# Performance work log

Hardware: AMD Instinct MI355X
Metric: run time of the kernel (lower is better)

Reference implementation:

```python
import jax, jax.numpy as jnp
import numpy as np

B, T, D = 2, 2048, 2048
N, K, H = 16, 8, 128  # heads, kv heads, head_dim
F = 8192              # ffn hidden


def _apply_rope(x, positions, max_wavelength=10000):
    # x: [B, L, heads, H]; positions: [B, L]
    half = x.shape[-1] // 2
    freq_exponents = (2.0 / x.shape[-1]) * jnp.arange(half, dtype=jnp.float32)
    timescale = max_wavelength ** freq_exponents
    radians = positions.astype(jnp.float32)[..., None] / timescale[None, None, :]
    radians = radians[..., None, :]  # [B, L, 1, half]
    sin, cos = jnp.sin(radians), jnp.cos(radians)
    x1, x2 = jnp.split(x, 2, axis=-1)
    return jnp.concatenate([x1 * cos - x2 * sin, x2 * cos + x1 * sin], axis=-1)


def _rms_norm(x, scale):
    var = jnp.mean(jnp.square(x), axis=-1, keepdims=True)
    return x * jax.lax.rsqrt(var + 1e-6) * (1 + scale)


def setup_inputs() -> dict:
    key = jax.random.key(0)
    ks = jax.random.split(key, 8)
    s = 0.02
    x = jax.random.normal(ks[0], (B, T, D), jnp.float32)
    positions = jnp.broadcast_to(jnp.arange(T, dtype=jnp.int32)[None, :], (B, T))
    causal = jnp.tril(jnp.ones((T, T), dtype=bool))
    attn_mask = jnp.broadcast_to(causal[None, None, :, :], (B, 1, T, T))
    return {
        "x": x,
        "positions": positions,
        "attn_mask": attn_mask,
        "w_q": jax.random.normal(ks[1], (N, D, H), jnp.float32) * s,
        "w_kv": jax.random.normal(ks[2], (2, K, D, H), jnp.float32) * s,
        "w_attn_vec": jax.random.normal(ks[3], (N, H, D), jnp.float32) * s,
        "scale_pre_attn": jax.random.normal(ks[4], (D,), jnp.float32) * s,
        "scale_pre_ffw": jax.random.normal(ks[5], (D,), jnp.float32) * s,
        "w_gating": jax.random.normal(ks[6], (2, D, F), jnp.float32) * s,
        "w_linear": jax.random.normal(ks[7], (F, D), jnp.float32) * s,
    }


def reference(x, positions, attn_mask, w_q, w_kv, w_attn_vec,
              scale_pre_attn, scale_pre_ffw, w_gating, w_linear):
    # pre-attention RMSNorm
    xn = _rms_norm(x, scale_pre_attn)

    # GQA projections
    q = jnp.einsum('BTD,NDH->BTNH', xn, w_q)
    kv = jnp.einsum('BSD,eKDH->eBSKH', xn, w_kv)
    k, v = kv[0], kv[1]

    q = _apply_rope(q, positions) * (H ** -0.5)
    k = _apply_rope(k, positions)

    G = N // K
    q = q.reshape(q.shape[0], q.shape[1], K, G, H)  # B T K G H
    logits = jnp.einsum('BTKGH,BSKH->BKGTS', q, k).astype(jnp.float32)
    big_neg = -2.3819763e38
    masked = jnp.where(attn_mask[:, :, None, :, :], logits, big_neg)
    probs = jax.nn.softmax(masked, axis=-1).astype(k.dtype)
    enc = jnp.einsum('BKGTS,BSKH->BTKGH', probs, v)
    enc = enc.reshape(enc.shape[0], enc.shape[1], N, H)
    attn_out = jnp.einsum('BTNH,NHD->BTD', enc, w_attn_vec)

    # residual + pre-FFN RMSNorm + GeGLU FFN
    residual = x + attn_out
    h = _rms_norm(residual, scale_pre_ffw)
    gate = jax.nn.gelu(jnp.dot(h, w_gating[0]))
    act = gate * jnp.dot(h, w_gating[1])
    out = residual + jnp.dot(act, w_linear)
    return out
```

## Files before the change

### kernel.cpp

```cpp
#include <hip/hip_runtime.h>
#include <hip/hip_bf16.h>


typedef __attribute__((ext_vector_type(8))) short bf16x8;
typedef __attribute__((ext_vector_type(4))) float f32x4;

#define GLP(p) ((const __attribute__((address_space(1))) void*)(p))
#define LDSP(p) ((__attribute__((address_space(3))) void*)(p))

__device__ __forceinline__ float bf2f(unsigned short h) {
  union { unsigned int u; float f; } v; v.u = ((unsigned int)h) << 16; return v.f;
}
__device__ __forceinline__ unsigned short f2bf(float f) {
  union { float f; unsigned int u; } v; v.f = f;
  unsigned int r = v.u + 0x7fffu + ((v.u >> 16) & 1u);
  return (unsigned short)(r >> 16);
}
__device__ __forceinline__ float gelu_f(float x) {
  float t = tanhf(0.7978845608028654f * (x + 0.044715f * x * x * x));
  return 0.5f * x * (1.f + t);
}

template <int IN_F32>
__global__ __launch_bounds__(256) void rmsnorm_kernel(const void* __restrict__ x_,
                                                      const float* __restrict__ scale,
                                                      unsigned short* __restrict__ out) {
  int row = blockIdx.x, tid = threadIdx.x;
  float f[8]; float ss = 0.f;
  if (IN_F32) {
    const float* xr = (const float*)x_ + (size_t)row * 2048 + tid * 8;
#pragma unroll
    for (int i = 0; i < 8; ++i) { f[i] = xr[i]; ss += f[i] * f[i]; }
  } else {
    const unsigned short* xr = (const unsigned short*)x_ + (size_t)row * 2048;
    bf16x8 xv = *(const bf16x8*)(xr + tid * 8);
#pragma unroll
    for (int i = 0; i < 8; ++i) { f[i] = bf2f((unsigned short)xv[i]); ss += f[i] * f[i]; }
  }
#pragma unroll
  for (int off = 32; off >= 1; off >>= 1) ss += __shfl_xor(ss, off);
  __shared__ float red[4];
  if ((tid & 63) == 0) red[tid >> 6] = ss;
  __syncthreads();
  ss = red[0] + red[1] + red[2] + red[3];
  float r = rsqrtf(ss * (1.f / 2048.f) + 1e-6f);
  const float* sv = scale + tid * 8;
  bf16x8 o;
#pragma unroll
  for (int i = 0; i < 8; ++i) o[i] = (short)f2bf(f[i] * r * (1.f + sv[i]));
  *(bf16x8*)(out + (size_t)row * 2048 + tid * 8) = o;
}

__global__ __launch_bounds__(256) void transpose_cast_kernel(const float* __restrict__ in,
                                                             unsigned short* __restrict__ out,
                                                             int R, int ldi, long ibs, long obs) {
  __shared__ float tile[32][33];
  int z = blockIdx.z;
  const float* ip = in + (size_t)z * ibs;
  unsigned short* op = out + (size_t)z * obs;
  int c0 = blockIdx.x * 32, r0 = blockIdx.y * 32;
  int tx = threadIdx.x, ty = threadIdx.y;
#pragma unroll
  for (int i = 0; i < 32; i += 8)
    tile[ty + i][tx] = ip[(size_t)(r0 + ty + i) * ldi + (c0 + tx)];
  __syncthreads();
#pragma unroll
  for (int i = 0; i < 32; i += 8)
    op[(size_t)(c0 + ty + i) * R + (r0 + tx)] = f2bf(tile[tx][ty + i]);
}

__global__ __launch_bounds__(256) void vtrans_kernel(const unsigned short* __restrict__ qkv,
                                                     unsigned short* __restrict__ vT) {
  __shared__ unsigned short tile[32][33];
  int z = blockIdx.z, bb = z >> 3, kh = z & 7;
  int s0 = blockIdx.x * 32, h0 = blockIdx.y * 32;
  int tx = threadIdx.x, ty = threadIdx.y;
  const unsigned short* ip = qkv + ((size_t)bb * 2048) * 4096 + 3072 + kh * 128;
  unsigned short* op = vT + (size_t)z * 128 * 2048;
#pragma unroll
  for (int i = 0; i < 32; i += 8)
    tile[ty + i][tx] = ip[(size_t)(s0 + ty + i) * 4096 + h0 + tx];
  __syncthreads();
#pragma unroll
  for (int i = 0; i < 32; i += 8)
    op[(size_t)(h0 + ty + i) * 2048 + s0 + tx] = tile[tx][ty + i];
}

template <int MODE, int OUT_F32, int ADD_F32>
__global__ __launch_bounds__(256, 2) void gemm_bt(const unsigned short* __restrict__ A, int lda,
                                                  const unsigned short* __restrict__ BT, int Kd,
                                                  int Ncols, void* __restrict__ out_,
                                                  const void* __restrict__ add_) {
  __shared__ unsigned short sA[128 * 32];
  __shared__ unsigned short sB[128 * 32];
  int tid = threadIdx.x;
  int lane = tid & 63, wave = tid >> 6;
  int quad = lane >> 4, l16 = lane & 15;
  int wr = (wave >> 1) * 64, wc = (wave & 1) * 64;
  long rowBase = (long)blockIdx.y * 128, colBase = (long)blockIdx.x * 128;
  f32x4 acc[4][4];
#pragma unroll
  for (int i = 0; i < 4; ++i)
#pragma unroll
    for (int j = 0; j < 4; ++j) acc[i][j] = (f32x4){0.f, 0.f, 0.f, 0.f};

  const unsigned short* Ag = A + (rowBase + (tid >> 2)) * (size_t)lda + (tid & 3) * 8;
  const unsigned short* Bg = BT + (colBase + (tid >> 2)) * (size_t)Kd + (tid & 3) * 8;
  unsigned short* sAw = sA + wave * 512;
  unsigned short* sBw = sB + wave * 512;

  for (int kt = 0; kt < Kd; kt += 32) {
    __syncthreads();
    __builtin_amdgcn_global_load_lds(GLP(Ag), LDSP(sAw), 16, 0, 0);
    __builtin_amdgcn_global_load_lds(GLP(Ag + (size_t)64 * lda), LDSP(sAw + 2048), 16, 0, 0);
    __builtin_amdgcn_global_load_lds(GLP(Bg), LDSP(sBw), 16, 0, 0);
    __builtin_amdgcn_global_load_lds(GLP(Bg + (size_t)64 * Kd), LDSP(sBw + 2048), 16, 0, 0);
    Ag += 32; Bg += 32;
    __syncthreads();
    bf16x8 af[4], bfr[4];
#pragma unroll
    for (int i = 0; i < 4; ++i) af[i] = *(const bf16x8*)(sA + (wr + i * 16 + l16) * 32 + quad * 8);
#pragma unroll
    for (int j = 0; j < 4; ++j) bfr[j] = *(const bf16x8*)(sB + (wc + j * 16 + l16) * 32 + quad * 8);
#pragma unroll
    for (int i = 0; i < 4; ++i)
#pragma unroll
      for (int j = 0; j < 4; ++j)
        acc[i][j] = __builtin_amdgcn_mfma_f32_16x16x32_bf16(af[i], bfr[j], acc[i][j], 0, 0, 0);
  }
  float* outf = (float*)out_;
  unsigned short* outb = (unsigned short*)out_;
  const float* addf = (const float*)add_;
  const unsigned short* addb = (const unsigned short*)add_;
#pragma unroll
  for (int i = 0; i < 4; ++i)
#pragma unroll
    for (int j = 0; j < 4; ++j)
#pragma unroll
      for (int r = 0; r < 4; ++r) {
        long row = rowBase + wr + i * 16 + quad * 4 + r;
        long col = colBase + wc + j * 16 + l16;
        long idx = row * (long)Ncols + col;
        float v = acc[i][j][r];
        if (MODE == 1) v += (ADD_F32 ? addf[idx] : bf2f(addb[idx]));
        if (OUT_F32) outf[idx] = v; else outb[idx] = f2bf(v);
      }
}

__global__ __launch_bounds__(256, 2) void gemm_gating(const unsigned short* __restrict__ A,
                                                      const unsigned short* __restrict__ BgT,
                                                      const unsigned short* __restrict__ BuT,
                                                      unsigned short* __restrict__ act,
                                                      long colOfs) {
  __shared__ unsigned short sA[128 * 32];
  __shared__ unsigned short sBg[128 * 32];
  __shared__ unsigned short sBu[128 * 32];
  int tid = threadIdx.x;
  int lane = tid & 63, wave = tid >> 6;
  int quad = lane >> 4, l16 = lane & 15;
  int wr = (wave >> 1) * 64, wc = (wave & 1) * 64;
  long rowBase = (long)blockIdx.y * 128, colBase = (long)blockIdx.x * 128;
  f32x4 gacc[4][4], uacc[4][4];
#pragma unroll
  for (int i = 0; i < 4; ++i)
#pragma unroll
    for (int j = 0; j < 4; ++j) {
      gacc[i][j] = (f32x4){0.f, 0.f, 0.f, 0.f};
      uacc[i][j] = (f32x4){0.f, 0.f, 0.f, 0.f};
    }

  const unsigned short* Ag  = A + (rowBase + (tid >> 2)) * (size_t)2048 + (tid & 3) * 8;
  const unsigned short* Bgg = BgT + (colBase + (tid >> 2)) * (size_t)2048 + (tid & 3) * 8;
  const unsigned short* Bug = BuT + (colBase + (tid >> 2)) * (size_t)2048 + (tid & 3) * 8;
  unsigned short* sAw = sA + wave * 512;
  unsigned short* sBgw = sBg + wave * 512;
  unsigned short* sBuw = sBu + wave * 512;

  for (int kt = 0; kt < 2048; kt += 32) {
    __syncthreads();
    __builtin_amdgcn_global_load_lds(GLP(Ag), LDSP(sAw), 16, 0, 0);
    __builtin_amdgcn_global_load_lds(GLP(Ag + (size_t)64 * 2048), LDSP(sAw + 2048), 16, 0, 0);
    __builtin_amdgcn_global_load_lds(GLP(Bgg), LDSP(sBgw), 16, 0, 0);
    __builtin_amdgcn_global_load_lds(GLP(Bgg + (size_t)64 * 2048), LDSP(sBgw + 2048), 16, 0, 0);
    __builtin_amdgcn_global_load_lds(GLP(Bug), LDSP(sBuw), 16, 0, 0);
    __builtin_amdgcn_global_load_lds(GLP(Bug + (size_t)64 * 2048), LDSP(sBuw + 2048), 16, 0, 0);
    Ag += 32; Bgg += 32; Bug += 32;
    __syncthreads();
    bf16x8 af[4], bg[4], bu[4];
#pragma unroll
    for (int i = 0; i < 4; ++i) af[i] = *(const bf16x8*)(sA + (wr + i * 16 + l16) * 32 + quad * 8);
#pragma unroll
    for (int j = 0; j < 4; ++j) bg[j] = *(const bf16x8*)(sBg + (wc + j * 16 + l16) * 32 + quad * 8);
#pragma unroll
    for (int j = 0; j < 4; ++j) bu[j] = *(const bf16x8*)(sBu + (wc + j * 16 + l16) * 32 + quad * 8);
#pragma unroll
    for (int i = 0; i < 4; ++i)
#pragma unroll
      for (int j = 0; j < 4; ++j) {
        gacc[i][j] = __builtin_amdgcn_mfma_f32_16x16x32_bf16(af[i], bg[j], gacc[i][j], 0, 0, 0);
        uacc[i][j] = __builtin_amdgcn_mfma_f32_16x16x32_bf16(af[i], bu[j], uacc[i][j], 0, 0, 0);
      }
  }
#pragma unroll
  for (int i = 0; i < 4; ++i)
#pragma unroll
    for (int j = 0; j < 4; ++j)
#pragma unroll
      for (int r = 0; r < 4; ++r) {
        long row = rowBase + wr + i * 16 + quad * 4 + r;
        long col = colBase + wc + j * 16 + l16;
        act[row * 8192 + colOfs + col] = f2bf(gelu_f(gacc[i][j][r]) * uacc[i][j][r]);
      }
}

__global__ __launch_bounds__(256) void rope_kernel(unsigned short* __restrict__ qkv,
                                                   const int* __restrict__ pos) {
  int gid = blockIdx.x * 256 + threadIdx.x;
  int hp = gid & 63;
  int rh = gid >> 6;
  int row = rh / 24;
  int head = rh - row * 24;
  float p = (float)pos[row];
  long cb; float sc;
  if (head < 16) { cb = (long)head * 128; sc = 0.08838834764831845f; }
  else { cb = 2048 + (long)(head - 16) * 128; sc = 1.f; }
  unsigned short* ptr = qkv + (long)row * 4096 + cb;
  float inv = exp2f(-(float)hp * (13.287712379549449f / 64.f));
  float ang = p * inv;
  float s = sinf(ang), c = cosf(ang);
  float x1 = bf2f(ptr[hp]), x2 = bf2f(ptr[hp + 64]);
  ptr[hp]      = f2bf((x1 * c - x2 * s) * sc);
  ptr[hp + 64] = f2bf((x2 * c + x1 * s) * sc);
}

__global__ __launch_bounds__(256, 2) void attn_kernel(const unsigned short* __restrict__ qkv,
                                                      const unsigned short* __restrict__ vT,
                                                      unsigned short* __restrict__ enc) {
  extern __shared__ char smem[];
  unsigned short* sK = (unsigned short*)smem;
  unsigned short* sVT = sK + 64 * 128;
  float* sS = (float*)(smem + 32768);
  unsigned short* sP = (unsigned short*)(smem + 32768 + 16896);
  float* sM = (float*)(smem + 32768 + 16896 + 9216);
  float* sL = sM + 64;
  float* sAl = sL + 64;

  int qt = blockIdx.x, n = blockIdx.y, b = blockIdx.z;
  int tid = threadIdx.x, lane = tid & 63, w = tid >> 6;
  int quad = lane >> 4, l16 = lane & 15;
  int kh = n >> 1;
  long rowQ = (long)b * 2048 + (long)qt * 64;

  bf16x8 qf[4];
  {
    const unsigned short* qp = qkv + (rowQ + w * 16 + l16) * 4096 + n * 128 + quad * 8;
#pragma unroll
    for (int ks = 0; ks < 4; ++ks) qf[ks] = *(const bf16x8*)(qp + ks * 32);
  }
  if (tid < 64) { sM[tid] = -1e30f; sL[tid] = 0.f; }
  f32x4 oacc[8];
#pragma unroll
  for (int t = 0; t < 8; ++t) oacc[t] = (f32x4){0.f, 0.f, 0.f, 0.f};

  int srow = tid >> 2, cg = tid & 3;

  for (int st = 0; st <= qt; ++st) {
    __syncthreads();
#pragma unroll
    for (int it = 0; it < 4; ++it) {
      int idx = it * 256 + tid;
      int r = idx >> 4, c = idx & 15;
      bf16x8 kv8 = *(const bf16x8*)(qkv + ((long)b * 2048 + st * 64 + r) * 4096 + 2048 + kh * 128 + c * 8);
      *(bf16x8*)(sK + r * 128 + ((c ^ (r & 7)) * 8)) = kv8;
    }
#pragma unroll
    for (int it = 0; it < 4; ++it) {
      int idx = it * 256 + tid;
      int h = idx >> 3, c = idx & 7;
      bf16x8 vv8 = *(const bf16x8*)(vT + ((long)(b * 8 + kh) * 128 + h) * 2048 + st * 64 + c * 8);
      *(bf16x8*)(sVT + h * 64 + ((c ^ (h & 7)) * 8)) = vv8;
    }
    __syncthreads();

    f32x4 sacc[4];
#pragma unroll
    for (int nt = 0; nt < 4; ++nt) sacc[nt] = (f32x4){0.f, 0.f, 0.f, 0.f};
#pragma unroll
    for (int ks = 0; ks < 4; ++ks)
#pragma unroll
      for (int nt = 0; nt < 4; ++nt) {
        int r = nt * 16 + l16;
        bf16x8 kf = *(const bf16x8*)(sK + r * 128 + (((ks * 4 + quad) ^ (r & 7)) * 8));
        sacc[nt] = __builtin_amdgcn_mfma_f32_16x16x32_bf16(qf[ks], kf, sacc[nt], 0, 0, 0);
      }
#pragma unroll
    for (int nt = 0; nt < 4; ++nt)
#pragma unroll
      for (int r = 0; r < 4; ++r)
        sS[(w * 16 + quad * 4 + r) * 66 + nt * 16 + l16] = sacc[nt][r];
    __syncthreads();

    float vals[16];
    int tglob = qt * 64 + srow;
    float mx = -1e30f;
#pragma unroll
    for (int j = 0; j < 16; ++j) {
      int col = cg * 16 + j;
      float v = sS[srow * 66 + col];
      if (st * 64 + col > tglob) v = -1e30f;
      vals[j] = v;
      mx = fmaxf(mx, v);
    }
    mx = fmaxf(mx, __shfl_xor(mx, 1));
    mx = fmaxf(mx, __shfl_xor(mx, 2));
    float m_old = sM[srow], l_old = sL[srow];
    float m_new = fmaxf(m_old, mx);
    float alpha = __expf(m_old - m_new);
    float sum = 0.f;
#pragma unroll
    for (int j = 0; j < 16; ++j) { vals[j] = __expf(vals[j] - m_new); sum += vals[j]; }
    sum += __shfl_xor(sum, 1);
    sum += __shfl_xor(sum, 2);
    float l_new = alpha * l_old + sum;
    __syncthreads();

#pragma unroll
    for (int jj = 0; jj < 8; ++jj) {
      unsigned int pk = (unsigned int)f2bf(vals[2 * jj]) | ((unsigned int)f2bf(vals[2 * jj + 1]) << 16);
      *(unsigned int*)(sP + srow * 72 + cg * 16 + jj * 2) = pk;
    }
    if (cg == 0) { sM[srow] = m_new; sL[srow] = l_new; sAl[srow] = alpha; }
    __syncthreads();

#pragma unroll
    for (int r = 0; r < 4; ++r) {
      float al = sAl[w * 16 + quad * 4 + r];
#pragma unroll
      for (int nt = 0; nt < 8; ++nt) oacc[nt][r] *= al;
    }
#pragma unroll
    for (int ks = 0; ks < 2; ++ks) {
      bf16x8 pf = *(const bf16x8*)(sP + (w * 16 + l16) * 72 + ks * 32 + quad * 8);
#pragma unroll
      for (int nt = 0; nt < 8; ++nt) {
        int hh = nt * 16 + l16;
        bf16x8 vf = *(const bf16x8*)(sVT + hh * 64 + (((ks * 4 + quad) ^ (hh & 7)) * 8));
        oacc[nt] = __builtin_amdgcn_mfma_f32_16x16x32_bf16(pf, vf, oacc[nt], 0, 0, 0);
      }
    }
  }

#pragma unroll
  for (int r = 0; r < 4; ++r) {
    float invl = 1.f / sL[w * 16 + quad * 4 + r];
    long trow = rowQ + w * 16 + quad * 4 + r;
#pragma unroll
    for (int nt = 0; nt < 8; ++nt)
      enc[trow * 2048 + n * 128 + nt * 16 + l16] = f2bf(oacc[nt][r] * invl);
  }
}

extern "C" void kernel_launch(void* const* d_in, const int* in_sizes, int n_in,
                              void* d_out, int out_size, void* d_ws, size_t ws_size,
                              hipStream_t stream) {
  const float* x = (const float*)d_in[0];
  const int* positions = (const int*)d_in[1];
  const float* wq = (const float*)d_in[3];
  const float* wkv = (const float*)d_in[4];
  const float* wav = (const float*)d_in[5];
  const float* s_attn = (const float*)d_in[6];
  const float* s_ffw = (const float*)d_in[7];
  const float* wg = (const float*)d_in[8];
  const float* wl = (const float*)d_in[9];
  float* outp = (float*)d_out;

  char* ws = (char*)d_ws;
  size_t o = 0;
  unsigned short* XN = (unsigned short*)(ws + o);    o += (size_t)4096 * 2048 * 2;
  unsigned short* WQKVT = (unsigned short*)(ws + o); o += (size_t)4096 * 2048 * 2;
  unsigned short* WAVT = (unsigned short*)(ws + o);  o += (size_t)2048 * 2048 * 2;
  unsigned short* WGT = (unsigned short*)(ws + o);   o += (size_t)8192 * 2048 * 2;
  unsigned short* QKV = (unsigned short*)(ws + o);   o += (size_t)4096 * 4096 * 2;
  unsigned short* VTb = (unsigned short*)(ws + o);   o += (size_t)16 * 128 * 2048 * 2;
  unsigned short* ACT = (unsigned short*)(ws + o);   o += (size_t)4096 * 8192 * 2;
  unsigned short* ENC = WQKVT;
  unsigned short* RES = QKV;
  unsigned short* HB = XN;

  dim3 b256(256), bT(32, 8);

  rmsnorm_kernel<1><<<4096, b256, 0, stream>>>(x, s_attn, XN);

  transpose_cast_kernel<<<dim3(4, 64, 16), bT, 0, stream>>>(wq, WQKVT, 2048, 128, 262144L, 262144L);
  transpose_cast_kernel<<<dim3(4, 64, 8), bT, 0, stream>>>(wkv, WQKVT + (size_t)2048 * 2048, 2048, 128, 262144L, 262144L);
  transpose_cast_kernel<<<dim3(4, 64, 8), bT, 0, stream>>>(wkv + (size_t)8 * 262144, WQKVT + (size_t)3072 * 2048, 2048, 128, 262144L, 262144L);
  transpose_cast_kernel<<<dim3(64, 64, 1), bT, 0, stream>>>(wav, WAVT, 2048, 2048, 0L, 0L);

  gemm_bt<0, 0, 0><<<dim3(32, 32), b256, 0, stream>>>(XN, 2048, WQKVT, 2048, 4096, QKV, nullptr);

  vtrans_kernel<<<dim3(64, 4, 16), bT, 0, stream>>>(QKV, VTb);

  rope_kernel<<<24576, b256, 0, stream>>>(QKV, positions);

  attn_kernel<<<dim3(32, 16, 2), b256, 59648, stream>>>(QKV, VTb, ENC);

  gemm_bt<1, 0, 1><<<dim3(16, 32), b256, 0, stream>>>(ENC, 2048, WAVT, 2048, 2048, RES, x);

  rmsnorm_kernel<0><<<4096, b256, 0, stream>>>(RES, s_ffw, HB);

  for (int half = 0; half < 2; ++half) {
    long f0 = (long)half * 4096;
    transpose_cast_kernel<<<dim3(128, 64, 1), bT, 0, stream>>>(wg + f0, WGT, 2048, 8192, 0L, 0L);
    transpose_cast_kernel<<<dim3(128, 64, 1), bT, 0, stream>>>(wg + (size_t)2048 * 8192 + f0,
                                                               WGT + (size_t)4096 * 2048, 2048, 8192, 0L, 0L);
    gemm_gating<<<dim3(32, 32), b256, 0, stream>>>(HB, WGT, WGT + (size_t)4096 * 2048, ACT, f0);
  }

  transpose_cast_kernel<<<dim3(64, 256, 1), bT, 0, stream>>>(wl, WGT, 8192, 2048, 0L, 0L);
  gemm_bt<1, 1, 0><<<dim3(16, 32), b256, 0, stream>>>(ACT, 8192, WGT, 8192, 2048, outp, RES);
}
```

Baseline: 1.155 ms.

## Double-buffer LDS tiles in GEMM kernels to overlap loads with MFMA

Both the generic GEMM and the fused gating GEMM now use two LDS buffers per operand. Each block issues the first tile's global-to-LDS load up front. Inside the loop it starts the async load of tile k+1 into the spare buffer before running the MFMAs on tile k, and it drops one of the two barriers per iteration. This is meant to hide global memory latency behind matrix compute, at the cost of doubled LDS per block (48KB for the gating kernel), which could limit occupancy.

```diff
diff --git a/kernel.cpp b/kernel.cpp
--- a/kernel.cpp
+++ b/kernel.cpp
@@ -91,8 +91,8 @@
                                                   const unsigned short* __restrict__ BT, int Kd,
                                                   int Ncols, void* __restrict__ out_,
                                                   const void* __restrict__ add_) {
-  __shared__ unsigned short sA[128 * 32];
-  __shared__ unsigned short sB[128 * 32];
+  __shared__ unsigned short sA0[128 * 32], sA1[128 * 32];
+  __shared__ unsigned short sB0[128 * 32], sB1[128 * 32];
   int tid = threadIdx.x;
   int lane = tid & 63, wave = tid >> 6;
   int quad = lane >> 4, l16 = lane & 15;
@@ -106,27 +106,38 @@
 
   const unsigned short* Ag = A + (rowBase + (tid >> 2)) * (size_t)lda + (tid & 3) * 8;
   const unsigned short* Bg = BT + (colBase + (tid >> 2)) * (size_t)Kd + (tid & 3) * 8;
-  unsigned short* sAw = sA + wave * 512;
-  unsigned short* sBw = sB + wave * 512;
-
-  for (int kt = 0; kt < Kd; kt += 32) {
-    __syncthreads();
-    __builtin_amdgcn_global_load_lds(GLP(Ag), LDSP(sAw), 16, 0, 0);
-    __builtin_amdgcn_global_load_lds(GLP(Ag + (size_t)64 * lda), LDSP(sAw + 2048), 16, 0, 0);
-    __builtin_amdgcn_global_load_lds(GLP(Bg), LDSP(sBw), 16, 0, 0);
-    __builtin_amdgcn_global_load_lds(GLP(Bg + (size_t)64 * Kd), LDSP(sBw + 2048), 16, 0, 0);
-    Ag += 32; Bg += 32;
-    __syncthreads();
+  int wofs = wave * 512;
+
+  __builtin_amdgcn_global_load_lds(GLP(Ag), LDSP(sA0 + wofs), 16, 0, 0);
+  __builtin_amdgcn_global_load_lds(GLP(Ag + (size_t)64 * lda), LDSP(sA0 + 2048 + wofs), 16, 0, 0);
+  __builtin_amdgcn_global_load_lds(GLP(Bg), LDSP(sB0 + wofs), 16, 0, 0);
+  __builtin_amdgcn_global_load_lds(GLP(Bg + (size_t)64 * Kd), LDSP(sB0 + 2048 + wofs), 16, 0, 0);
+  Ag += 32; Bg += 32;
+
+  unsigned short *curA = sA0, *nxtA = sA1, *curB = sB0, *nxtB = sB1;
+  int nIter = Kd >> 5;
+  for (int k = 0; k < nIter; ++k) {
+    __syncthreads();
+    if (k + 1 < nIter) {
+      __builtin_amdgcn_global_load_lds(GLP(Ag), LDSP(nxtA + wofs), 16, 0, 0);
+      __builtin_amdgcn_global_load_lds(GLP(Ag + (size_t)64 * lda), LDSP(nxtA + 2048 + wofs), 16, 0, 0);
+      __builtin_amdgcn_global_load_lds(GLP(Bg), LDSP(nxtB + wofs), 16, 0, 0);
+      __builtin_amdgcn_global_load_lds(GLP(Bg + (size_t)64 * Kd), LDSP(nxtB + 2048 + wofs), 16, 0, 0);
+      Ag += 32; Bg += 32;
+    }
     bf16x8 af[4], bfr[4];
 #pragma unroll
-    for (int i = 0; i < 4; ++i) af[i] = *(const bf16x8*)(sA + (wr + i * 16 + l16) * 32 + quad * 8);
-#pragma unroll
-    for (int j = 0; j < 4; ++j) bfr[j] = *(const bf16x8*)(sB + (wc + j * 16 + l16) * 32 + quad * 8);
+    for (int i = 0; i < 4; ++i) af[i] = *(const bf16x8*)(curA + (wr + i * 16 + l16) * 32 + quad * 8);
+#pragma unroll
+    for (int j = 0; j < 4; ++j) bfr[j] = *(const bf16x8*)(curB + (wc + j * 16 + l16) * 32 + quad * 8);
 #pragma unroll
     for (int i = 0; i < 4; ++i)
 #pragma unroll
       for (int j = 0; j < 4; ++j)
         acc[i][j] = __builtin_amdgcn_mfma_f32_16x16x32_bf16(af[i], bfr[j], acc[i][j], 0, 0, 0);
+    unsigned short* t;
+    t = curA; curA = nxtA; nxtA = t;
+    t = curB; curB = nxtB; nxtB = t;
   }
   float* outf = (float*)out_;
   unsigned short* outb = (unsigned short*)out_;
@@ -152,9 +163,9 @@
                                                       const unsigned short* __restrict__ BuT,
                                                       unsigned short* __restrict__ act,
                                                       long colOfs) {
-  __shared__ unsigned short sA[128 * 32];
-  __shared__ unsigned short sBg[128 * 32];
-  __shared__ unsigned short sBu[128 * 32];
+  __shared__ unsigned short sA0[128 * 32], sA1[128 * 32];
+  __shared__ unsigned short sG0[128 * 32], sG1[128 * 32];
+  __shared__ unsigned short sU0[128 * 32], sU1[128 * 32];
   int tid = threadIdx.x;
   int lane = tid & 63, wave = tid >> 6;
   int quad = lane >> 4, l16 = lane & 15;
@@ -172,27 +183,35 @@
   const unsigned short* Ag  = A + (rowBase + (tid >> 2)) * (size_t)2048 + (tid & 3) * 8;
   const unsigned short* Bgg = BgT + (colBase + (tid >> 2)) * (size_t)2048 + (tid & 3) * 8;
   const unsigned short* Bug = BuT + (colBase + (tid >> 2)) * (size_t)2048 + (tid & 3) * 8;
-  unsigned short* sAw = sA + wave * 512;
-  unsigned short* sBgw = sBg + wave * 512;
-  unsigned short* sBuw = sBu + wave * 512;
-
-  for (int kt = 0; kt < 2048; kt += 32) {
-    __syncthreads();
-    __builtin_amdgcn_global_load_lds(GLP(Ag), LDSP(sAw), 16, 0, 0);
-    __builtin_amdgcn_global_load_lds(GLP(Ag + (size_t)64 * 2048), LDSP(sAw + 2048), 16, 0, 0);
-    __builtin_amdgcn_global_load_lds(GLP(Bgg), LDSP(sBgw), 16, 0, 0);
-    __builtin_amdgcn_global_load_lds(GLP(Bgg + (size_t)64 * 2048), LDSP(sBgw + 2048), 16, 0, 0);
-    __builtin_amdgcn_global_load_lds(GLP(Bug), LDSP(sBuw), 16, 0, 0);
-    __builtin_amdgcn_global_load_lds(GLP(Bug + (size_t)64 * 2048), LDSP(sBuw + 2048), 16, 0, 0);
-    Ag += 32; Bgg += 32; Bug += 32;
-    __syncthreads();
+  int wofs = wave * 512;
+
+  __builtin_amdgcn_global_load_lds(GLP(Ag), LDSP(sA0 + wofs), 16, 0, 0);
+  __builtin_amdgcn_global_load_lds(GLP(Ag + (size_t)64 * 2048), LDSP(sA0 + 2048 + wofs), 16, 0, 0);
+  __builtin_amdgcn_global_load_lds(GLP(Bgg), LDSP(sG0 + wofs), 16, 0, 0);
+  __builtin_amdgcn_global_load_lds(GLP(Bgg + (size_t)64 * 2048), LDSP(sG0 + 2048 + wofs), 16, 0, 0);
+  __builtin_amdgcn_global_load_lds(GLP(Bug), LDSP(sU0 + wofs), 16, 0, 0);
+  __builtin_amdgcn_global_load_lds(GLP(Bug + (size_t)64 * 2048), LDSP(sU0 + 2048 + wofs), 16, 0, 0);
+  Ag += 32; Bgg += 32; Bug += 32;
+
+  unsigned short *curA = sA0, *nxtA = sA1, *curG = sG0, *nxtG = sG1, *curU = sU0, *nxtU = sU1;
+  for (int k = 0; k < 64; ++k) {
+    __syncthreads();
+    if (k + 1 < 64) {
+      __builtin_amdgcn_global_load_lds(GLP(Ag), LDSP(nxtA + wofs), 16, 0, 0);
+      __builtin_amdgcn_global_load_lds(GLP(Ag + (size_t)64 * 2048), LDSP(nxtA + 2048 + wofs), 16, 0, 0);
+      __builtin_amdgcn_global_load_lds(GLP(Bgg), LDSP(nxtG + wofs), 16, 0, 0);
+      __builtin_amdgcn_global_load_lds(GLP(Bgg + (size_t)64 * 2048), LDSP(nxtG + 2048 + wofs), 16, 0, 0);
+      __builtin_amdgcn_global_load_lds(GLP(Bug), LDSP(nxtU + wofs), 16, 0, 0);
+      __builtin_amdgcn_global_load_lds(GLP(Bug + (size_t)64 * 2048), LDSP(nxtU + 2048 + wofs), 16, 0, 0);
+      Ag += 32; Bgg += 32; Bug += 32;
+    }
     bf16x8 af[4], bg[4], bu[4];
 #pragma unroll
-    for (int i = 0; i < 4; ++i) af[i] = *(const bf16x8*)(sA + (wr + i * 16 + l16) * 32 + quad * 8);
-#pragma unroll
-    for (int j = 0; j < 4; ++j) bg[j] = *(const bf16x8*)(sBg + (wc + j * 16 + l16) * 32 + quad * 8);
-#pragma unroll
-    for (int j = 0; j < 4; ++j) bu[j] = *(const bf16x8*)(sBu + (wc + j * 16 + l16) * 32 + quad * 8);
+    for (int i = 0; i < 4; ++i) af[i] = *(const bf16x8*)(curA + (wr + i * 16 + l16) * 32 + quad * 8);
+#pragma unroll
+    for (int j = 0; j < 4; ++j) bg[j] = *(const bf16x8*)(curG + (wc + j * 16 + l16) * 32 + quad * 8);
+#pragma unroll
+    for (int j = 0; j < 4; ++j) bu[j] = *(const bf16x8*)(curU + (wc + j * 16 + l16) * 32 + quad * 8);
 #pragma unroll
     for (int i = 0; i < 4; ++i)
 #pragma unroll
@@ -200,6 +219,10 @@
         gacc[i][j] = __builtin_amdgcn_mfma_f32_16x16x32_bf16(af[i], bg[j], gacc[i][j], 0, 0, 0);
         uacc[i][j] = __builtin_amdgcn_mfma_f32_16x16x32_bf16(af[i], bu[j], uacc[i][j], 0, 0, 0);
       }
+    unsigned short* t;
+    t = curA; curA = nxtA; nxtA = t;
+    t = curG; curG = nxtG; nxtG = t;
+    t = curU; curU = nxtU; nxtU = t;
   }
 #pragma unroll
   for (int i = 0; i < 4; ++i)
```

Result: faster. 1.092 ms (-5.5%).
